# Kernel optimization log

Measured on AMD Instinct MI355X. Metric: run time of the kernel, lower is better.

## Reference

```python
import jax, jax.numpy as jnp
import numpy as np

N = 100000   # nodes
E = 640000   # edges
H = 8        # attention heads
C = 16       # hidden_channels (per-head out dim)
IN = 4       # in_channels
G = 64       # graphs in the batch
NE = 2       # num_experts
HC = H * C   # 128 = concat feature width
SLOPE = 0.2  # GATConv leaky_relu negative slope


def _p(k, shape):
    return 0.1 * jax.random.normal(k, shape, jnp.float32)


def setup_inputs() -> dict:
    key = jax.random.key(0)
    ks = jax.random.split(key, 32)
    inp = {
        "x": jax.random.normal(ks[0], (N, IN), jnp.float32),
        "edge_index": jax.random.randint(ks[1], (2, E), 0, N),
        "edge_attr": jax.random.normal(ks[2], (E, 1), jnp.float32),
        "batch": jnp.sort(jax.random.randint(ks[3], (N,), 0, G)),
    }
    i = 4
    for l, d in zip((1, 2, 3), (IN, HC, HC)):
        inp[f"w{l}"] = _p(ks[i], (d, HC)); i += 1      # node lin
        inp[f"as{l}"] = _p(ks[i], (H, C)); i += 1      # att_src
        inp[f"ad{l}"] = _p(ks[i], (H, C)); i += 1      # att_dst
        inp[f"we{l}"] = _p(ks[i], (1, HC)); i += 1     # lin_edge
        inp[f"ae{l}"] = _p(ks[i], (H, C)); i += 1      # att_edge
        inp[f"b{l}"] = jnp.zeros((HC,), jnp.float32)
    inp["fw1"] = _p(ks[i], (HC, 4 * C)); inp["fb1"] = jnp.zeros((4 * C,), jnp.float32)
    inp["fw2"] = _p(ks[i + 1], (4 * C, NE)); inp["fb2"] = jnp.zeros((NE,), jnp.float32)
    return inp


def gat_layer(x, src, dst, eattr, w, a_s, a_d, we, a_e, b):
    """PyG GATConv (concat=True, edge_dim=1): gather-attend-segment_softmax-scatter."""
    n = x.shape[0]
    h = (x @ w).reshape(n, H, C)                       # [N,H,C]
    alpha_src = jnp.sum(h * a_s, axis=-1)              # [N,H]
    alpha_dst = jnp.sum(h * a_d, axis=-1)              # [N,H]
    ef = (eattr @ we).reshape(-1, H, C)                # [E,H,C]
    alpha_e = jnp.sum(ef * a_e, axis=-1)               # [E,H]
    alpha = jax.nn.leaky_relu(alpha_src[src] + alpha_dst[dst] + alpha_e, SLOPE)
    # segment softmax over incoming edges of each dst node
    m = jax.lax.stop_gradient(jax.ops.segment_max(alpha, dst, num_segments=n))
    m = jnp.where(jnp.isfinite(m), m, 0.0)
    ex = jnp.exp(alpha - m[dst])
    den = jax.ops.segment_sum(ex, dst, num_segments=n)
    alpha = ex / (den[dst] + 1e-16)
    out = jax.ops.segment_sum(h[src] * alpha[:, :, None], dst, num_segments=n)
    return out.reshape(n, HC) + b


def add_self_loops_mean(src, dst, eattr, n):
    """add_self_loops(fill_value='mean'): self-loop attr = mean of incoming edge attrs."""
    cnt = jax.ops.segment_sum(jnp.ones(src.shape, eattr.dtype), dst, num_segments=n)
    loop = jax.ops.segment_sum(eattr, dst, num_segments=n) / jnp.maximum(cnt, 1.0)[:, None]
    idx = jnp.arange(n, dtype=src.dtype)
    return (jnp.concatenate([src, idx]), jnp.concatenate([dst, idx]),
            jnp.concatenate([eattr, loop], axis=0))


def reference(x, edge_index, edge_attr, batch,
              w1, as1, ad1, we1, ae1, b1,
              w2, as2, ad2, we2, ae2, b2,
              w3, as3, ad3, we3, ae3, b3,
              fw1, fb1, fw2, fb2):
    src, dst = edge_index[0], edge_index[1]
    # conv1: add_self_loops=False
    h = jax.nn.relu(gat_layer(x, src, dst, edge_attr, w1, as1, ad1, we1, ae1, b1))
    # conv2/conv3: default add_self_loops=True with fill_value='mean'
    s2, d2, e2 = add_self_loops_mean(src, dst, edge_attr, x.shape[0])
    h = jax.nn.relu(gat_layer(h, s2, d2, e2, w2, as2, ad2, we2, ae2, b2))
    h = jax.nn.relu(gat_layer(h, s2, d2, e2, w3, as3, ad3, we3, ae3, b3))
    # global mean pool over `batch`
    gsum = jax.ops.segment_sum(h, batch, num_segments=G)
    cnt = jax.ops.segment_sum(jnp.ones((h.shape[0],), h.dtype), batch, num_segments=G)
    emb = gsum / jnp.maximum(cnt, 1.0)[:, None]
    gh = jax.nn.relu(emb @ fw1 + fb1)
    return gh @ fw2 + fb2
```

## Files before the change

kernel.cpp:

```cpp
#include <hip/hip_runtime.h>
#include <hip/hip_bf16.h>
#include <math.h>

#define NHEAD 8
#define CDIM 16
#define HCDIM 128
#define NGRAPH 64
#define WEXT 144
#define SWPAD 136

typedef __attribute__((ext_vector_type(8))) short short8;
typedef __attribute__((ext_vector_type(4))) float f32x4;
typedef __attribute__((ext_vector_type(2))) float f32x2;

static __device__ __forceinline__ unsigned short f2bf(float f) {
    unsigned u = __float_as_uint(f);
    unsigned r = (u + 0x7FFF + ((u >> 16) & 1)) >> 16;
    return (unsigned short)r;
}
static __device__ __forceinline__ float bf2f(unsigned short s) {
    return __uint_as_float(((unsigned)s) << 16);
}
static __device__ __forceinline__ f32x2 bfpair(unsigned u) {
    return (f32x2){ __uint_as_float(u << 16), __uint_as_float(u & 0xffff0000u) };
}


__global__ void setup0(int* __restrict__ deg,
                       float* __restrict__ gsum,
                       const float* __restrict__ w2, const float* __restrict__ w3,
                       unsigned short* __restrict__ wt2, unsigned short* __restrict__ wt3,
                       const float* __restrict__ we1, const float* __restrict__ ae1,
                       const float* __restrict__ we2, const float* __restrict__ ae2,
                       const float* __restrict__ we3, const float* __restrict__ ae3,
                       float* __restrict__ kc,
                       const float* __restrict__ as2, const float* __restrict__ ad2,
                       const float* __restrict__ as3, const float* __restrict__ ad3,
                       const float* __restrict__ w1,
                       const float* __restrict__ as1, const float* __restrict__ ad1,
                       float* __restrict__ wastab, float* __restrict__ wadtab,
                       const int* __restrict__ batch, int* __restrict__ gstart, int n) {
    int i = blockIdx.x * 256 + threadIdx.x;
    if (i < n) deg[i] = 0;
    if (i < NGRAPH * HCDIM) gsum[i] = 0.f;
    if (i < WEXT * HCDIM) {
        int nn = i >> 7, k = i & 127;
        float v2, v3;
        if (nn < HCDIM) {
            v2 = w2[k * HCDIM + nn];
            v3 = w3[k * HCDIM + nn];
        } else if (nn < HCDIM + NHEAD) {
            int h = nn - HCDIM;
            float s2 = 0.f, s3 = 0.f;
#pragma unroll
            for (int c = 0; c < CDIM; ++c) {
                s2 += w2[k * HCDIM + h * CDIM + c] * as2[h * CDIM + c];
                s3 += w3[k * HCDIM + h * CDIM + c] * as3[h * CDIM + c];
            }
            v2 = s2; v3 = s3;
        } else {
            int h = nn - HCDIM - NHEAD;
            float s2 = 0.f, s3 = 0.f;
#pragma unroll
            for (int c = 0; c < CDIM; ++c) {
                s2 += w2[k * HCDIM + h * CDIM + c] * ad2[h * CDIM + c];
                s3 += w3[k * HCDIM + h * CDIM + c] * ad3[h * CDIM + c];
            }
            v2 = s2; v3 = s3;
        }
        wt2[nn * HCDIM + k] = f2bf(v2);
        wt3[nn * HCDIM + k] = f2bf(v3);
    }
    if (i < 24) {
        int l = i >> 3, h = i & 7;
        const float* we = (l == 0) ? we1 : ((l == 1) ? we2 : we3);
        const float* ae = (l == 0) ? ae1 : ((l == 1) ? ae2 : ae3);
        float s = 0.f;
        for (int c = 0; c < CDIM; ++c) s += we[h * CDIM + c] * ae[h * CDIM + c];
        kc[i] = s;
    }
    if (i >= 18560 && i <= 18560 + NGRAPH) {
        int g = i - 18560;
        int lo = 0, hi = n;
        while (lo < hi) {
            int mid = (lo + hi) >> 1;
            if (batch[mid] < g) lo = mid + 1; else hi = mid;
        }
        gstart[g] = lo;
    }
    if (i >= 18700 && i < 18732) {
        int t = i - 18700;
        int k = t >> 3, h = t & 7;
        float ss = 0.f, sd = 0.f;
#pragma unroll
        for (int c = 0; c < CDIM; ++c) {
            ss += w1[k * HCDIM + h * CDIM + c] * as1[h * CDIM + c];
            sd += w1[k * HCDIM + h * CDIM + c] * ad1[h * CDIM + c];
        }
        wastab[t] = ss;
        wadtab[t] = sd;
    }
}

__global__ void count_deg(const int* __restrict__ dst, int* __restrict__ deg,
                          int* __restrict__ erank, int E) {
    int e = blockIdx.x * 256 + threadIdx.x;
    if (e >= E) return;
    erank[e] = atomicAdd(&deg[dst[e]], 1);
}

__global__ __launch_bounds__(512) void block_sum(const int* __restrict__ deg,
                                                 int* __restrict__ bsum, int n) {
    __shared__ int s[512];
    int i = blockIdx.x * 512 + threadIdx.x;
    s[threadIdx.x] = (i < n) ? deg[i] : 0;
    __syncthreads();
    for (int off = 256; off > 0; off >>= 1) {
        if (threadIdx.x < off) s[threadIdx.x] += s[threadIdx.x + off];
        __syncthreads();
    }
    if (threadIdx.x == 0) bsum[blockIdx.x] = s[0];
}

__global__ __launch_bounds__(512) void scan_final2(const int* __restrict__ deg,
                                                   const int* __restrict__ bsum, int nb,
                                                   int* __restrict__ eoff, int n) {
    __shared__ int ls[512];
    __shared__ int s[512];
    const int t = threadIdx.x;
    ls[t] = (t < nb) ? bsum[t] : 0;
    int i = blockIdx.x * 512 + t;
    s[t] = (i < n) ? deg[i] : 0;
    __syncthreads();
    for (int off = 1; off < 512; off <<= 1) {
        int a1 = (t >= off) ? ls[t - off] : 0;
        int a2 = (t >= off) ? s[t - off] : 0;
        __syncthreads();
        ls[t] += a1; s[t] += a2;
        __syncthreads();
    }
    int base = (blockIdx.x > 0) ? ls[blockIdx.x - 1] : 0;
    if (i < n) eoff[i + 1] = base + s[t];
    if (i == 0) eoff[0] = 0;
}

__global__ void scatter_edges(const int* __restrict__ src, const int* __restrict__ dst,
                              const float* __restrict__ eattr,
                              const int* __restrict__ eoff,
                              const int* __restrict__ erank,
                              int2* __restrict__ epack, int E) {
    int e = blockIdx.x * 256 + threadIdx.x;
    if (e >= E) return;
    int p = eoff[dst[e]] + erank[e];
    epack[p] = make_int2(src[e], __float_as_int(eattr[e]));
}


__global__ __launch_bounds__(256) void gat_aggregate1(
    const float* __restrict__ x,
    const int2*  __restrict__ epack,
    const int*   __restrict__ eoff,
    const float* __restrict__ w1,
    const float* __restrict__ wastab,
    const float* __restrict__ wadtab,
    const float* __restrict__ kc,
    const float* __restrict__ bias,
    unsigned short* __restrict__ outbf,
    int n) {
    const int lane = threadIdx.x & 63;
    const int l16 = lane & 15;
    int nid = ((blockIdx.x * 256 + threadIdx.x) >> 6) * 4 + (lane >> 4);
    if (nid >= n) return;
    const int h = l16 >> 1;
    const int c0 = l16 * 8;

    float was0 = wastab[0 * NHEAD + h], was1_ = wastab[1 * NHEAD + h];
    float was2 = wastab[2 * NHEAD + h], was3 = wastab[3 * NHEAD + h];
    float wad0 = wadtab[0 * NHEAD + h], wad1_ = wadtab[1 * NHEAD + h];
    float wad2 = wadtab[2 * NHEAD + h], wad3 = wadtab[3 * NHEAD + h];

    f32x4 xd = *(const f32x4*)(x + (((unsigned)nid) << 2));
    const float adst_h = xd[0] * wad0 + xd[1] * wad1_ + xd[2] * wad2 + xd[3] * wad3;
    const float k_h = kc[h];
    const int e0 = eoff[nid], e1 = eoff[nid + 1];

    float den = 0.f;
    f32x4 acc4 = (f32x4){0.f, 0.f, 0.f, 0.f};

    if (e0 < e1) {
        int2 ep[4];
#pragma unroll
        for (int j = 0; j < 4; ++j) {
            int idx = e0 + j; idx = (idx < e1) ? idx : (e1 - 1);
            ep[j] = epack[idx];
        }
        for (int base = e0; base < e1; base += 4) {
            int2 epn[4];
#pragma unroll
            for (int j = 0; j < 4; ++j) {
                int idx = base + 4 + j; idx = (idx < e1) ? idx : (e1 - 1);
                epn[j] = epack[idx];
            }
            f32x4 xs[4];
#pragma unroll
            for (int j = 0; j < 4; ++j)
                xs[j] = *(const f32x4*)(x + (((unsigned)ep[j].x) << 2));
#pragma unroll
            for (int j = 0; j < 4; ++j) {
                bool valid = (base + j < e1);
                float as_e = xs[j][0] * was0 + xs[j][1] * was1_ +
                             xs[j][2] * was2 + xs[j][3] * was3;
                float a = as_e + adst_h + __int_as_float(ep[j].y) * k_h;
                a = (a > 0.f) ? a : 0.2f * a;
                float w = valid ? __expf(a) : 0.f;
                den += w;
                acc4 += xs[j] * w;
            }
#pragma unroll
            for (int j = 0; j < 4; ++j) ep[j] = epn[j];
        }
    }

    float inv = 1.f / (den + 1e-16f);
    short8 o;
#pragma unroll
    for (int c = 0; c < 8; ++c) {
        float oc = acc4[0] * w1[0 * HCDIM + c0 + c] + acc4[1] * w1[1 * HCDIM + c0 + c] +
                   acc4[2] * w1[2 * HCDIM + c0 + c] + acc4[3] * w1[3 * HCDIM + c0 + c];
        oc = fmaxf(oc * inv + bias[c0 + c], 0.f);
        o[c] = (short)f2bf(oc);
    }
    *(short8*)(outbf + (long)nid * HCDIM + c0) = o;
}


__global__ __launch_bounds__(256) void gemm_mfma(const unsigned short* __restrict__ A,
                                                 const unsigned short* __restrict__ Wt,
                                                 unsigned short* __restrict__ Ybf,
                                                 float* __restrict__ asrcn,
                                                 float* __restrict__ adstn, int n) {
    __shared__ unsigned short sW[WEXT][SWPAD];
    for (int i = threadIdx.x; i < WEXT * 16; i += 256) {
        int r = i >> 4, c = (i & 15) << 3;
        *(short8*)&sW[r][c] = *(const short8*)(Wt + r * HCDIM + c);
    }
    __syncthreads();

    const int wave = threadIdx.x >> 6;
    const int lane = threadIdx.x & 63;
    const int quad = lane >> 4;
    const int l16  = lane & 15;
    const int rowbase = (blockIdx.x * 8 + wave * 2) * 16;

    f32x4 acc[2][9];
#pragma unroll
    for (int r = 0; r < 2; ++r)
#pragma unroll
        for (int t = 0; t < 9; ++t) acc[r][t] = (f32x4){0.f, 0.f, 0.f, 0.f};

#pragma unroll
    for (int kb = 0; kb < HCDIM; kb += 32) {
        short8 a[2];
#pragma unroll
        for (int r = 0; r < 2; ++r) {
            int row = rowbase + r * 16 + l16;
            row = (row < n) ? row : (n - 1);
            a[r] = *(const short8*)(A + (long)row * HCDIM + kb + quad * 8);
        }
#pragma unroll
        for (int nt = 0; nt < 9; ++nt) {
            short8 b = *(const short8*)(&sW[nt * 16 + l16][kb + quad * 8]);
#pragma unroll
            for (int r = 0; r < 2; ++r)
                acc[r][nt] = __builtin_amdgcn_mfma_f32_16x16x32_bf16(a[r], b, acc[r][nt], 0, 0, 0);
        }
    }

#pragma unroll
    for (int r = 0; r < 2; ++r) {
#pragma unroll
        for (int reg = 0; reg < 4; ++reg) {
            int row = rowbase + r * 16 + quad * 4 + reg;
            if (row < n) {
                unsigned short* yp = Ybf + (long)row * HCDIM + l16;
#pragma unroll
                for (int nt = 0; nt < 8; ++nt) yp[nt * 16] = f2bf(acc[r][nt][reg]);
                float cv = acc[r][8][reg];
                if (l16 < 8) asrcn[row * NHEAD + l16] = cv;
                else         adstn[row * NHEAD + (l16 - 8)] = cv;
            }
        }
    }
}


__global__ __launch_bounds__(256) void gat_aggregate(
    const unsigned short* __restrict__ hlin,
    const float* __restrict__ asrc,
    const float* __restrict__ adst,
    const int2*  __restrict__ epack,
    const int*   __restrict__ eoff,
    const float* __restrict__ kc,
    const float* __restrict__ bias,
    unsigned short* __restrict__ out,
    int n, int use_loop) {
    const int lane = threadIdx.x & 63;
    const int l16 = lane & 15;
    int nid = ((blockIdx.x * 256 + threadIdx.x) >> 6) * 4 + (lane >> 4);
    if (nid >= n) return;
    const int h = l16 >> 1;
    const int c0 = l16 * 8;

    const float adst_h = adst[nid * NHEAD + h];
    const float k_h = kc[h];
    const int e0 = eoff[nid], e1 = eoff[nid + 1];

    float den = 0.f, sume = 0.f;
    f32x2 acc[4];
#pragma unroll
    for (int p = 0; p < 4; ++p) acc[p] = (f32x2){0.f, 0.f};

    if (e0 < e1) {
        int2 ep[4];
#pragma unroll
        for (int j = 0; j < 4; ++j) {
            int idx = e0 + j; idx = (idx < e1) ? idx : (e1 - 1);
            ep[j] = epack[idx];
        }
        for (int base = e0; base < e1; base += 4) {
            int2 epn[4];
#pragma unroll
            for (int j = 0; j < 4; ++j) {
                int idx = base + 4 + j; idx = (idx < e1) ? idx : (e1 - 1);
                epn[j] = epack[idx];
            }
            float av[4]; uint4 hv[4];
#pragma unroll
            for (int j = 0; j < 4; ++j) {
                av[j] = *(asrc + (((unsigned)ep[j].x) << 3) + h);
                hv[j] = *(const uint4*)(hlin + (((unsigned)ep[j].x) << 7) + c0);
            }
#pragma unroll
            for (int j = 0; j < 4; ++j) {
                bool valid = (base + j < e1);
                float ea = __int_as_float(ep[j].y);
                float a = av[j] + adst_h + ea * k_h;
                a = (a > 0.f) ? a : 0.2f * a;
                float w = valid ? __expf(a) : 0.f;
                sume += valid ? ea : 0.f;
                den += w;
                acc[0] += bfpair(hv[j].x) * w;
                acc[1] += bfpair(hv[j].y) * w;
                acc[2] += bfpair(hv[j].z) * w;
                acc[3] += bfpair(hv[j].w) * w;
            }
#pragma unroll
            for (int j = 0; j < 4; ++j) ep[j] = epn[j];
        }
    }

    if (use_loop) {
        float fl = sume / fmaxf((float)(e1 - e0), 1.f);
        float a = asrc[nid * NHEAD + h] + adst_h + fl * k_h;
        a = (a > 0.f) ? a : 0.2f * a;
        float w = __expf(a);
        uint4 hv = *(const uint4*)(hlin + (((unsigned)nid) << 7) + c0);
        den += w;
        acc[0] += bfpair(hv.x) * w;
        acc[1] += bfpair(hv.y) * w;
        acc[2] += bfpair(hv.z) * w;
        acc[3] += bfpair(hv.w) * w;
    }

    float inv = 1.f / (den + 1e-16f);
    short8 o;
#pragma unroll
    for (int c = 0; c < 8; ++c) {
        float oc = fmaxf(acc[c >> 1][c & 1] * inv + bias[c0 + c], 0.f);
        o[c] = (short)f2bf(oc);
    }
    *(short8*)(out + (long)nid * HCDIM + c0) = o;
}


__global__ __launch_bounds__(128) void pool_seg(const unsigned short* __restrict__ H,
                                                const int* __restrict__ gstart,
                                                float* __restrict__ gsum) {
    const int c = threadIdx.x;
    const int g = blockIdx.x >> 3;
    const int chunk = blockIdx.x & 7;
    int s0 = gstart[g], s1 = gstart[g + 1];
    int len = s1 - s0;
    if (len <= 0) return;
    int cl = (len + 7) >> 3;
    int i0 = s0 + chunk * cl;
    int i1 = min(i0 + cl, s1);
    if (i0 >= i1) return;
    float acc = 0.f;
    int i = i0;
    for (; i + 4 <= i1; i += 4) {
        float v0 = bf2f(H[(long)i * HCDIM + c]);
        float v1 = bf2f(H[(long)(i + 1) * HCDIM + c]);
        float v2 = bf2f(H[(long)(i + 2) * HCDIM + c]);
        float v3 = bf2f(H[(long)(i + 3) * HCDIM + c]);
        acc += (v0 + v1) + (v2 + v3);
    }
    for (; i < i1; ++i) acc += bf2f(H[(long)i * HCDIM + c]);
    atomicAdd(&gsum[g * HCDIM + c], acc);
}

__global__ __launch_bounds__(64) void mlp_kernel(const float* __restrict__ gsum,
                                                 const int* __restrict__ gstart,
                                                 const float* __restrict__ fw1,
                                                 const float* __restrict__ fb1,
                                                 const float* __restrict__ fw2,
                                                 const float* __restrict__ fb2,
                                                 float* __restrict__ out) {
    const int g = blockIdx.x;
    const int j = threadIdx.x;
    __shared__ float emb[HCDIM];
    __shared__ float gh[64];
    int cnt = gstart[g + 1] - gstart[g];
    float invc = 1.f / fmaxf((float)cnt, 1.f);
    emb[j] = gsum[g * HCDIM + j] * invc;
    emb[j + 64] = gsum[g * HCDIM + 64 + j] * invc;
    __syncthreads();
    float a = fb1[j];
    for (int k = 0; k < HCDIM; ++k) a += emb[k] * fw1[k * 64 + j];
    gh[j] = fmaxf(a, 0.f);
    __syncthreads();
    if (j < 2) {
        float o = fb2[j];
        for (int k = 0; k < 64; ++k) o += gh[k] * fw2[k * 2 + j];
        out[g * 2 + j] = o;
    }
}


extern "C" void kernel_launch(void* const* d_in, const int* in_sizes, int n_in,
                              void* d_out, int out_size, void* d_ws, size_t ws_size,
                              hipStream_t stream) {
    const float* x     = (const float*)d_in[0];
    const int*   eidx  = (const int*)d_in[1];
    const float* eattr = (const float*)d_in[2];
    const int*   batch = (const int*)d_in[3];
    const float* w1  = (const float*)d_in[4];
    const float* as1 = (const float*)d_in[5];
    const float* ad1 = (const float*)d_in[6];
    const float* we1 = (const float*)d_in[7];
    const float* ae1 = (const float*)d_in[8];
    const float* b1  = (const float*)d_in[9];
    const float* w2  = (const float*)d_in[10];
    const float* as2 = (const float*)d_in[11];
    const float* ad2 = (const float*)d_in[12];
    const float* we2 = (const float*)d_in[13];
    const float* ae2 = (const float*)d_in[14];
    const float* b2  = (const float*)d_in[15];
    const float* w3  = (const float*)d_in[16];
    const float* as3 = (const float*)d_in[17];
    const float* ad3 = (const float*)d_in[18];
    const float* we3 = (const float*)d_in[19];
    const float* ae3 = (const float*)d_in[20];
    const float* b3  = (const float*)d_in[21];
    const float* fw1 = (const float*)d_in[22];
    const float* fb1 = (const float*)d_in[23];
    const float* fw2 = (const float*)d_in[24];
    const float* fb2 = (const float*)d_in[25];

    const int N = in_sizes[3];
    const int E = in_sizes[2];
    const int* src = eidx;
    const int* dst = eidx + E;

    char* p = (char*)d_ws;
    auto alloc = [&](size_t bytes) {
        void* r = (void*)p;
        p += (bytes + 255) & ~(size_t)255;
        return r;
    };
    unsigned short* Abf = (unsigned short*)alloc((size_t)N * HCDIM * 2);
    unsigned short* Bbf = (unsigned short*)alloc((size_t)N * HCDIM * 2);
    float* asrcA  = (float*)alloc((size_t)N * NHEAD * 4);
    float* adstA  = (float*)alloc((size_t)N * NHEAD * 4);
    float* asrcB  = (float*)alloc((size_t)N * NHEAD * 4);
    float* adstB  = (float*)alloc((size_t)N * NHEAD * 4);
    int*   deg    = (int*)alloc((size_t)N * 4);
    int*   eoff   = (int*)alloc((size_t)(N + 1) * 4);
    int*   erank  = (int*)alloc((size_t)E * 4);
    int2*  epack  = (int2*)alloc((size_t)E * 8);
    int*   bsum   = (int*)alloc(((size_t)(N + 511) / 512) * 4);
    float* kc     = (float*)alloc(24 * 4);
    int*   gstart = (int*)alloc((NGRAPH + 1) * 4);
    float* gsum   = (float*)alloc(NGRAPH * HCDIM * 4);
    float* wastab = (float*)alloc(32 * 4);
    float* wadtab = (float*)alloc(32 * 4);
    unsigned short* wt2 = (unsigned short*)alloc(WEXT * HCDIM * 2);
    unsigned short* wt3 = (unsigned short*)alloc(WEXT * HCDIM * 2);

    const int NB = (N + 255) / 256;
    const int NB512 = (N + 511) / 512;
    const int EB = (E + 255) / 256;
    const int AGG_BLOCKS = (((N + 3) / 4) * 64 + 255) / 256;
    const int GEMM_BLOCKS = (N + 127) / 128;

    setup0<<<NB, 256, 0, stream>>>(deg, gsum,
                                   w2, w3, wt2, wt3,
                                   we1, ae1, we2, ae2, we3, ae3, kc,
                                   as2, ad2, as3, ad3,
                                   w1, as1, ad1, wastab, wadtab,
                                   batch, gstart, N);
    count_deg<<<EB, 256, 0, stream>>>(dst, deg, erank, E);
    block_sum<<<NB512, 512, 0, stream>>>(deg, bsum, N);
    scan_final2<<<NB512, 512, 0, stream>>>(deg, bsum, NB512, eoff, N);
    scatter_edges<<<EB, 256, 0, stream>>>(src, dst, eattr, eoff, erank, epack, E);

    gat_aggregate1<<<AGG_BLOCKS, 256, 0, stream>>>(x, epack, eoff, w1, wastab, wadtab,
                                                   kc + 0, b1, Bbf, N);
    gemm_mfma<<<GEMM_BLOCKS, 256, 0, stream>>>(Bbf, wt2, Abf, asrcB, adstB, N);
    gat_aggregate<<<AGG_BLOCKS, 256, 0, stream>>>(Abf, asrcB, adstB, epack, eoff,
                                                  kc + 8, b2, Bbf, N, 1);
    gemm_mfma<<<GEMM_BLOCKS, 256, 0, stream>>>(Bbf, wt3, Abf, asrcA, adstA, N);
    gat_aggregate<<<AGG_BLOCKS, 256, 0, stream>>>(Abf, asrcA, adstA, epack, eoff,
                                                  kc + 16, b3, Bbf, N, 1);

    pool_seg<<<NGRAPH * 8, 128, 0, stream>>>(Bbf, gstart, gsum);
    mlp_kernel<<<NGRAPH, 64, 0, stream>>>(gsum, gstart, fw1, fb1, fw2, fb2, (float*)d_out);
}
```

Measured before the change: 327.8 us.

## Interleave alpha_src into feature rows, single-pass lookback scan, fuse pool with MLP

The GEMM now writes each node's per-head source attention scores right after its 128 bf16 features, using a 144-element row stride. The aggregation gather then fetches the features and the score from one row instead of two separate arrays. The two-kernel block scan becomes a single kernel where each block spin-waits on flags published by earlier blocks, and the pooling kernel runs the MLP in whichever block finishes a graph last, detected with an atomic counter. Together these remove two kernel launches and one scattered gather per edge. In exchange the rows are wider, and the spin-wait relies on all 196 blocks being co-resident.

```diff
diff --git a/kernel.cpp b/kernel.cpp
--- a/kernel.cpp
+++ b/kernel.cpp
@@ -8,6 +8,7 @@
 #define NGRAPH 64
 #define WEXT 144
 #define SWPAD 136
+#define YSTRIDE 144
 
 typedef __attribute__((ext_vector_type(8))) short short8;
 typedef __attribute__((ext_vector_type(4))) float f32x4;
@@ -39,7 +40,8 @@
                        const float* __restrict__ w1,
                        const float* __restrict__ as1, const float* __restrict__ ad1,
                        float* __restrict__ wastab, float* __restrict__ wadtab,
-                       const int* __restrict__ batch, int* __restrict__ gstart, int n) {
+                       const int* __restrict__ batch, int* __restrict__ gstart,
+                       int* __restrict__ bflag, int* __restrict__ gcnt, int n) {
     int i = blockIdx.x * 256 + threadIdx.x;
     if (i < n) deg[i] = 0;
     if (i < NGRAPH * HCDIM) gsum[i] = 0.f;
@@ -100,6 +102,8 @@
         wastab[t] = ss;
         wadtab[t] = sd;
     }
+    if (i >= 19000 && i < 19256) bflag[i - 19000] = 0;
+    if (i >= 19300 && i < 19300 + NGRAPH) gcnt[i - 19300] = 0;
 }
 
 __global__ void count_deg(const int* __restrict__ dst, int* __restrict__ deg,
@@ -109,37 +113,35 @@
     erank[e] = atomicAdd(&deg[dst[e]], 1);
 }
 
-__global__ __launch_bounds__(512) void block_sum(const int* __restrict__ deg,
-                                                 int* __restrict__ bsum, int n) {
+__global__ __launch_bounds__(512) void scan_lookback(const int* __restrict__ deg,
+                                                     int* __restrict__ bflag,
+                                                     int* __restrict__ eoff, int n) {
     __shared__ int s[512];
-    int i = blockIdx.x * 512 + threadIdx.x;
-    s[threadIdx.x] = (i < n) ? deg[i] : 0;
+    __shared__ int ls[512];
+    const int t = threadIdx.x;
+    const int b = blockIdx.x;
+    int i = b * 512 + t;
+    s[t] = (i < n) ? deg[i] : 0;
+    __syncthreads();
+    for (int off = 1; off < 512; off <<= 1) {
+        int a = (t >= off) ? s[t - off] : 0;
+        __syncthreads();
+        s[t] += a;
+        __syncthreads();
+    }
+    if (t == 0) atomicExch(&bflag[b], s[511] + 1);
+    ls[t] = 0;
+    if (t < b) {
+        int v;
+        do { v = atomicAdd(&bflag[t], 0); } while (v == 0);
+        ls[t] = v - 1;
+    }
     __syncthreads();
     for (int off = 256; off > 0; off >>= 1) {
-        if (threadIdx.x < off) s[threadIdx.x] += s[threadIdx.x + off];
+        if (t < off) ls[t] += ls[t + off];
         __syncthreads();
     }
-    if (threadIdx.x == 0) bsum[blockIdx.x] = s[0];
-}
-
-__global__ __launch_bounds__(512) void scan_final2(const int* __restrict__ deg,
-                                                   const int* __restrict__ bsum, int nb,
-                                                   int* __restrict__ eoff, int n) {
-    __shared__ int ls[512];
-    __shared__ int s[512];
-    const int t = threadIdx.x;
-    ls[t] = (t < nb) ? bsum[t] : 0;
-    int i = blockIdx.x * 512 + t;
-    s[t] = (i < n) ? deg[i] : 0;
-    __syncthreads();
-    for (int off = 1; off < 512; off <<= 1) {
-        int a1 = (t >= off) ? ls[t - off] : 0;
-        int a2 = (t >= off) ? s[t - off] : 0;
-        __syncthreads();
-        ls[t] += a1; s[t] += a2;
-        __syncthreads();
-    }
-    int base = (blockIdx.x > 0) ? ls[blockIdx.x - 1] : 0;
+    int base = ls[0];
     if (i < n) eoff[i + 1] = base + s[t];
     if (i == 0) eoff[0] = 0;
 }
@@ -237,7 +239,6 @@
 __global__ __launch_bounds__(256) void gemm_mfma(const unsigned short* __restrict__ A,
                                                  const unsigned short* __restrict__ Wt,
                                                  unsigned short* __restrict__ Ybf,
-                                                 float* __restrict__ asrcn,
                                                  float* __restrict__ adstn, int n) {
     __shared__ unsigned short sW[WEXT][SWPAD];
     for (int i = threadIdx.x; i < WEXT * 16; i += 256) {
@@ -282,11 +283,11 @@
         for (int reg = 0; reg < 4; ++reg) {
             int row = rowbase + r * 16 + quad * 4 + reg;
             if (row < n) {
-                unsigned short* yp = Ybf + (long)row * HCDIM + l16;
+                unsigned short* yp = Ybf + (long)row * YSTRIDE + l16;
 #pragma unroll
                 for (int nt = 0; nt < 8; ++nt) yp[nt * 16] = f2bf(acc[r][nt][reg]);
                 float cv = acc[r][8][reg];
-                if (l16 < 8) asrcn[row * NHEAD + l16] = cv;
+                if (l16 < 8) ((float*)(Ybf + (long)row * YSTRIDE + HCDIM))[l16] = cv;
                 else         adstn[row * NHEAD + (l16 - 8)] = cv;
             }
         }
@@ -296,7 +297,6 @@
 
 __global__ __launch_bounds__(256) void gat_aggregate(
     const unsigned short* __restrict__ hlin,
-    const float* __restrict__ asrc,
     const float* __restrict__ adst,
     const int2*  __restrict__ epack,
     const int*   __restrict__ eoff,
@@ -337,8 +337,9 @@
             float av[4]; uint4 hv[4];
 #pragma unroll
             for (int j = 0; j < 4; ++j) {
-                av[j] = *(asrc + (((unsigned)ep[j].x) << 3) + h);
-                hv[j] = *(const uint4*)(hlin + (((unsigned)ep[j].x) << 7) + c0);
+                unsigned rb = ((unsigned)ep[j].x) * YSTRIDE;
+                av[j] = ((const float*)(hlin + rb + HCDIM))[h];
+                hv[j] = *(const uint4*)(hlin + rb + c0);
             }
 #pragma unroll
             for (int j = 0; j < 4; ++j) {
@@ -360,11 +361,12 @@
     }
 
     if (use_loop) {
+        unsigned rb = ((unsigned)nid) * YSTRIDE;
         float fl = sume / fmaxf((float)(e1 - e0), 1.f);
-        float a = asrc[nid * NHEAD + h] + adst_h + fl * k_h;
+        float a = ((const float*)(hlin + rb + HCDIM))[h] + adst_h + fl * k_h;
         a = (a > 0.f) ? a : 0.2f * a;
         float w = __expf(a);
-        uint4 hv = *(const uint4*)(hlin + (((unsigned)nid) << 7) + c0);
+        uint4 hv = *(const uint4*)(hlin + rb + c0);
         den += w;
         acc[0] += bfpair(hv.x) * w;
         acc[1] += bfpair(hv.y) * w;
@@ -383,56 +385,64 @@
 }
 
 
-__global__ __launch_bounds__(128) void pool_seg(const unsigned short* __restrict__ H,
+__global__ __launch_bounds__(128) void pool_mlp(const unsigned short* __restrict__ H,
                                                 const int* __restrict__ gstart,
-                                                float* __restrict__ gsum) {
+                                                float* __restrict__ gsum,
+                                                int* __restrict__ gcnt,
+                                                const float* __restrict__ fw1,
+                                                const float* __restrict__ fb1,
+                                                const float* __restrict__ fw2,
+                                                const float* __restrict__ fb2,
+                                                float* __restrict__ out) {
     const int c = threadIdx.x;
     const int g = blockIdx.x >> 3;
     const int chunk = blockIdx.x & 7;
     int s0 = gstart[g], s1 = gstart[g + 1];
     int len = s1 - s0;
-    if (len <= 0) return;
-    int cl = (len + 7) >> 3;
-    int i0 = s0 + chunk * cl;
-    int i1 = min(i0 + cl, s1);
-    if (i0 >= i1) return;
-    float acc = 0.f;
-    int i = i0;
-    for (; i + 4 <= i1; i += 4) {
-        float v0 = bf2f(H[(long)i * HCDIM + c]);
-        float v1 = bf2f(H[(long)(i + 1) * HCDIM + c]);
-        float v2 = bf2f(H[(long)(i + 2) * HCDIM + c]);
-        float v3 = bf2f(H[(long)(i + 3) * HCDIM + c]);
-        acc += (v0 + v1) + (v2 + v3);
-    }
-    for (; i < i1; ++i) acc += bf2f(H[(long)i * HCDIM + c]);
-    atomicAdd(&gsum[g * HCDIM + c], acc);
-}
-
-__global__ __launch_bounds__(64) void mlp_kernel(const float* __restrict__ gsum,
-                                                 const int* __restrict__ gstart,
-                                                 const float* __restrict__ fw1,
-                                                 const float* __restrict__ fb1,
-                                                 const float* __restrict__ fw2,
-                                                 const float* __restrict__ fb2,
-                                                 float* __restrict__ out) {
-    const int g = blockIdx.x;
-    const int j = threadIdx.x;
+    if (len > 0) {
+        int cl = (len + 7) >> 3;
+        int i0 = s0 + chunk * cl;
+        int i1 = min(i0 + cl, s1);
+        if (i0 < i1) {
+            float acc = 0.f;
+            int i = i0;
+            for (; i + 4 <= i1; i += 4) {
+                float v0 = bf2f(H[(long)i * HCDIM + c]);
+                float v1 = bf2f(H[(long)(i + 1) * HCDIM + c]);
+                float v2 = bf2f(H[(long)(i + 2) * HCDIM + c]);
+                float v3 = bf2f(H[(long)(i + 3) * HCDIM + c]);
+                acc += (v0 + v1) + (v2 + v3);
+            }
+            for (; i < i1; ++i) acc += bf2f(H[(long)i * HCDIM + c]);
+            atomicAdd(&gsum[g * HCDIM + c], acc);
+        }
+    }
+    __syncthreads();
+    __shared__ int lastf;
+    if (c == 0) {
+        __threadfence();
+        int d = atomicAdd(&gcnt[g], 1);
+        lastf = (d == 7);
+    }
+    __syncthreads();
+    if (!lastf) return;
+
     __shared__ float emb[HCDIM];
     __shared__ float gh[64];
-    int cnt = gstart[g + 1] - gstart[g];
-    float invc = 1.f / fmaxf((float)cnt, 1.f);
-    emb[j] = gsum[g * HCDIM + j] * invc;
-    emb[j + 64] = gsum[g * HCDIM + 64 + j] * invc;
-    __syncthreads();
-    float a = fb1[j];
-    for (int k = 0; k < HCDIM; ++k) a += emb[k] * fw1[k * 64 + j];
-    gh[j] = fmaxf(a, 0.f);
-    __syncthreads();
-    if (j < 2) {
-        float o = fb2[j];
-        for (int k = 0; k < 64; ++k) o += gh[k] * fw2[k * 2 + j];
-        out[g * 2 + j] = o;
+    __threadfence();
+    float invc = 1.f / fmaxf((float)len, 1.f);
+    emb[c] = atomicAdd(&gsum[g * HCDIM + c], 0.f) * invc;
+    __syncthreads();
+    if (c < 64) {
+        float a = fb1[c];
+        for (int k = 0; k < HCDIM; ++k) a += emb[k] * fw1[k * 64 + c];
+        gh[c] = fmaxf(a, 0.f);
+    }
+    __syncthreads();
+    if (c < 2) {
+        float o = fb2[c];
+        for (int k = 0; k < 64; ++k) o += gh[k] * fw2[k * 2 + c];
+        out[g * 2 + c] = o;
     }
 }
 
@@ -478,20 +488,19 @@
         p += (bytes + 255) & ~(size_t)255;
         return r;
     };
-    unsigned short* Abf = (unsigned short*)alloc((size_t)N * HCDIM * 2);
+    unsigned short* Abf = (unsigned short*)alloc((size_t)N * YSTRIDE * 2);
     unsigned short* Bbf = (unsigned short*)alloc((size_t)N * HCDIM * 2);
-    float* asrcA  = (float*)alloc((size_t)N * NHEAD * 4);
     float* adstA  = (float*)alloc((size_t)N * NHEAD * 4);
-    float* asrcB  = (float*)alloc((size_t)N * NHEAD * 4);
     float* adstB  = (float*)alloc((size_t)N * NHEAD * 4);
     int*   deg    = (int*)alloc((size_t)N * 4);
     int*   eoff   = (int*)alloc((size_t)(N + 1) * 4);
     int*   erank  = (int*)alloc((size_t)E * 4);
     int2*  epack  = (int2*)alloc((size_t)E * 8);
-    int*   bsum   = (int*)alloc(((size_t)(N + 511) / 512) * 4);
+    int*   bflag  = (int*)alloc(256 * 4);
     float* kc     = (float*)alloc(24 * 4);
     int*   gstart = (int*)alloc((NGRAPH + 1) * 4);
     float* gsum   = (float*)alloc(NGRAPH * HCDIM * 4);
+    int*   gcnt   = (int*)alloc(NGRAPH * 4);
     float* wastab = (float*)alloc(32 * 4);
     float* wadtab = (float*)alloc(32 * 4);
     unsigned short* wt2 = (unsigned short*)alloc(WEXT * HCDIM * 2);
@@ -508,21 +517,20 @@
                                    we1, ae1, we2, ae2, we3, ae3, kc,
                                    as2, ad2, as3, ad3,
                                    w1, as1, ad1, wastab, wadtab,
-                                   batch, gstart, N);
+                                   batch, gstart, bflag, gcnt, N);
     count_deg<<<EB, 256, 0, stream>>>(dst, deg, erank, E);
-    block_sum<<<NB512, 512, 0, stream>>>(deg, bsum, N);
-    scan_final2<<<NB512, 512, 0, stream>>>(deg, bsum, NB512, eoff, N);
+    scan_lookback<<<NB512, 512, 0, stream>>>(deg, bflag, eoff, N);
     scatter_edges<<<EB, 256, 0, stream>>>(src, dst, eattr, eoff, erank, epack, E);
 
     gat_aggregate1<<<AGG_BLOCKS, 256, 0, stream>>>(x, epack, eoff, w1, wastab, wadtab,
                                                    kc + 0, b1, Bbf, N);
-    gemm_mfma<<<GEMM_BLOCKS, 256, 0, stream>>>(Bbf, wt2, Abf, asrcB, adstB, N);
-    gat_aggregate<<<AGG_BLOCKS, 256, 0, stream>>>(Abf, asrcB, adstB, epack, eoff,
+    gemm_mfma<<<GEMM_BLOCKS, 256, 0, stream>>>(Bbf, wt2, Abf, adstB, N);
+    gat_aggregate<<<AGG_BLOCKS, 256, 0, stream>>>(Abf, adstB, epack, eoff,
                                                   kc + 8, b2, Bbf, N, 1);
-    gemm_mfma<<<GEMM_BLOCKS, 256, 0, stream>>>(Bbf, wt3, Abf, asrcA, adstA, N);
-    gat_aggregate<<<AGG_BLOCKS, 256, 0, stream>>>(Abf, asrcA, adstA, epack, eoff,
+    gemm_mfma<<<GEMM_BLOCKS, 256, 0, stream>>>(Bbf, wt3, Abf, adstA, N);
+    gat_aggregate<<<AGG_BLOCKS, 256, 0, stream>>>(Abf, adstA, epack, eoff,
                                                   kc + 16, b3, Bbf, N, 1);
 
-    pool_seg<<<NGRAPH * 8, 128, 0, stream>>>(Bbf, gstart, gsum);
-    mlp_kernel<<<NGRAPH, 64, 0, stream>>>(gsum, gstart, fw1, fb1, fw2, fb2, (float*)d_out);
-}
+    pool_mlp<<<NGRAPH * 8, 128, 0, stream>>>(Bbf, gstart, gsum, gcnt,
+                                             fw1, fb1, fw2, fb2, (float*)d_out);
+}
```

Result: slower. 340.8 us (+4.0%).
